# Performance work log

Hardware: AMD Instinct MI355X
Metric: run time of the kernel (lower is better)

Reference implementation:

```python
import jax, jax.numpy as jnp
import numpy as np

N = 50000      # nodes
DIM = 128      # feature dim
H = 4          # heads
C = DIM // H   # per-head channels
E = 800000     # edges (before self-loops)
LRELU_SLOPE = 0.2
LN_EPS = 1e-5


def setup_inputs() -> dict:
    key = jax.random.key(0)
    ks = jax.random.split(key, 12)
    def p(k, shape, scale=0.05):
        return jax.random.normal(k, shape, jnp.float32) * scale
    return {
        "x": jax.random.normal(ks[0], (N, DIM), jnp.float32),
        "edge_index": jax.random.randint(ks[1], (2, E), 0, N),
        "W1": p(ks[2], (DIM, DIM)), "b1": jnp.zeros((DIM,), jnp.float32),
        "att_src1": p(ks[3], (H, C)), "att_dst1": p(ks[4], (H, C)),
        "W2": p(ks[5], (DIM, DIM)), "b2": jnp.zeros((DIM,), jnp.float32),
        "att_src2": p(ks[6], (H, C)), "att_dst2": p(ks[7], (H, C)),
        "gate_W": p(ks[8], (2 * DIM, 2)), "gate_b": jnp.zeros((2,), jnp.float32),
        "ln_gamma": jnp.ones((DIM,), jnp.float32), "ln_beta": jnp.zeros((DIM,), jnp.float32),
    }


def _gat(x, src, dst, W, b, a_src, a_dst):
    # Linear transform, split heads: [N, H, C]
    h = (x @ W).reshape(-1, H, C)
    # Per-node attention logits per head: [N, H]
    e_src = jnp.einsum("nhc,hc->nh", h, a_src)
    e_dst = jnp.einsum("nhc,hc->nh", h, a_dst)
    # Per-edge logits (edge j->i: src=j, dst=i): [E, H]
    e = jax.nn.leaky_relu(e_src[src] + e_dst[dst], LRELU_SLOPE)
    # Segment softmax over edges sharing a destination (self-loops guarantee >=1 edge/node)
    m = jax.ops.segment_max(e, dst, num_segments=N)
    p = jnp.exp(e - m[dst])
    s = jax.ops.segment_sum(p, dst, num_segments=N)
    alpha = p / s[dst]                                   # [E, H]
    # Weighted scatter-add aggregation
    out = jax.ops.segment_sum(h[src] * alpha[..., None], dst, num_segments=N)
    return out.reshape(-1, H * C) + b                    # [N, DIM]


def reference(x, edge_index, W1, b1, att_src1, att_dst1, W2, b2, att_src2, att_dst2,
              gate_W, gate_b, ln_gamma, ln_beta):
    n = x.shape[0]
    loops = jnp.arange(n, dtype=edge_index.dtype)
    src = jnp.concatenate([edge_index[0], loops])  # PyG GATConv add_self_loops=True
    dst = jnp.concatenate([edge_index[1], loops])
    out1 = _gat(x, src, dst, W1, b1, att_src1, att_dst1)
    out2 = _gat(x, src, dst, W2, b2, att_src2, att_dst2)
    gate = jax.nn.softmax(jnp.concatenate([out1, out2], axis=-1) @ gate_W + gate_b, axis=-1)
    out = gate[:, 0:1] * out1 + gate[:, 1:2] * out2
    # residual + LayerNorm (dropout is identity in eval)
    y = x + out
    mu = jnp.mean(y, axis=-1, keepdims=True)
    var = jnp.var(y, axis=-1, keepdims=True)
    return (y - mu) * jax.lax.rsqrt(var + LN_EPS) * ln_gamma + ln_beta
```

## Files before the change

### kernel.cpp

```cpp
#include <hip/hip_runtime.h>
#include <hip/hip_bf16.h>


typedef unsigned short u16;
typedef __bf16 bf16x8 __attribute__((ext_vector_type(8)));
typedef float f32x4 __attribute__((ext_vector_type(4)));

#define LRELU_SLOPE 0.2f
#define LN_EPS 1e-5f
#define SH 8

__device__ __forceinline__ float bfbits(unsigned int hi_bits) {
    union { unsigned int i; float f; } v; v.i = hi_bits; return v.f;
}
__device__ __forceinline__ float bflo(unsigned int u) { return bfbits(u << 16); }
__device__ __forceinline__ float bfhi(unsigned int u) { return bfbits(u & 0xFFFF0000u); }
__device__ __forceinline__ u16 f2bf(float f) {
    union { float f; unsigned int i; } v; v.f = f;
    unsigned int lsb = (v.i >> 16) & 1u;
    v.i += 0x7FFFu + lsb;
    return (u16)(v.i >> 16);
}

__global__ void k_prep(const float* __restrict__ W1, const float* __restrict__ W2,
                       u16* __restrict__ wb, int* __restrict__ deg8,
                       int* __restrict__ gflag, int n) {
    int i = blockIdx.x * 256 + threadIdx.x;
    if (i < 32768) {
        int e = i & 7, chunk = i >> 3;
        int lane = chunk & 63, ks = (chunk >> 6) & 3, t = chunk >> 8;
        int r16 = lane & 15, quad = lane >> 4;
        int colp = t * 16 + r16;
        int k = quad * 8 + ks * 32 + e;
        float v = (colp < 128) ? W1[k * 128 + colp] : W2[k * 128 + (colp - 128)];
        wb[i] = f2bf(v);
    }
    if (i < n) {
#pragma unroll
        for (int x = 0; x < SH; x++) deg8[x * n + i] = 0;
    }
    if (i == 0) *gflag = 0;
}

__global__ __launch_bounds__(256) void k_cg(const float* __restrict__ x,
                                            const u16* __restrict__ wb,
                                            unsigned int* __restrict__ hbp, int n,
                                            const int* __restrict__ ei,
                                            int* __restrict__ deg8,
                                            unsigned int* __restrict__ pk,
                                            int E, int Gg) {
    __shared__ u16 lwb[32768];
    if ((int)blockIdx.x >= Gg) {
        int bid = (int)blockIdx.x - Gg;
#pragma unroll
        for (int it = 0; it < 4; it++) {
            int i = bid * 1024 + it * 256 + threadIdx.x;
            if (i < E) {
                int d = ei[E + i];
                int sh = (i >> 8) & (SH - 1);
                unsigned int r = (unsigned int)atomicAdd(&deg8[sh * n + d], 1);
                pk[i] = (r << 17) | (unsigned int)d;
            }
        }
        return;
    }
    {
        const uint4* g = (const uint4*)wb;
        uint4* l = (uint4*)lwb;
#pragma unroll
        for (int r = 0; r < 16; r++) l[r * 256 + threadIdx.x] = g[r * 256 + threadIdx.x];
    }
    __syncthreads();
    int wave = threadIdx.x >> 6, lane = threadIdx.x & 63;
    int quad = lane >> 4, r16 = lane & 15;
    const u16* bb = lwb + lane * 8;
    for (int strip = 0; strip < 2; strip++) {
        int row = blockIdx.x * 128 + strip * 64 + wave * 16 + r16;
        int arow = (row < n) ? row : n - 1;
        const float* xp = x + (size_t)arow * 128 + quad * 8;
        union { u16 u[8]; bf16x8 b; } ar;
        bf16x8 a[4];
#pragma unroll
        for (int ks = 0; ks < 4; ks++) {
            float4 lo = *(const float4*)(xp + ks * 32);
            float4 hi = *(const float4*)(xp + ks * 32 + 4);
            ar.u[0] = f2bf(lo.x); ar.u[1] = f2bf(lo.y); ar.u[2] = f2bf(lo.z); ar.u[3] = f2bf(lo.w);
            ar.u[4] = f2bf(hi.x); ar.u[5] = f2bf(hi.y); ar.u[6] = f2bf(hi.z); ar.u[7] = f2bf(hi.w);
            a[ks] = ar.b;
        }
        f32x4 acc[16];
#pragma unroll
        for (int t = 0; t < 16; t++) acc[t] = (f32x4){0.f, 0.f, 0.f, 0.f};
#pragma unroll
        for (int t = 0; t < 16; t++) {
#pragma unroll
            for (int ks = 0; ks < 4; ks++) {
                bf16x8 b = *(const bf16x8*)(bb + (t * 4 + ks) * 512);
                acc[t] = __builtin_amdgcn_mfma_f32_16x16x32_bf16(a[ks], b, acc[t], 0, 0, 0);
            }
        }
        int row0 = blockIdx.x * 128 + strip * 64 + wave * 16 + quad * 4;
#pragma unroll
        for (int t = 0; t < 8; t++) {
            int c = t * 16 + r16;
#pragma unroll
            for (int g = 0; g < 4; g++) {
                int gr = row0 + g;
                if (gr < n) {
                    unsigned int pv = ((unsigned int)f2bf(acc[t + 8][g]) << 16) | f2bf(acc[t][g]);
                    hbp[(size_t)gr * 128 + c] = pv;
                }
            }
        }
    }
}

__global__ void k_ss(int* __restrict__ deg8, int* __restrict__ offs,
                     int* __restrict__ bsum, int* __restrict__ gflag,
                     int nb, int n) {
    __shared__ int s[256];
    int t = threadIdx.x;
    int i = blockIdx.x * 256 + t;
    int d[SH];
    int v = 0;
    if (i < n) {
#pragma unroll
        for (int x = 0; x < SH; x++) { d[x] = deg8[x * n + i]; v += d[x]; }
    }
    s[t] = v;
    __syncthreads();
    for (int o = 1; o < 256; o <<= 1) {
        int u = (t >= o) ? s[t - o] : 0;
        __syncthreads();
        s[t] += u;
        __syncthreads();
    }
    int myinc = s[t];
    int total = s[255];
    if (t == 0) {
        bsum[blockIdx.x] = total;
        __threadfence();
        atomicAdd(gflag, 1);
        while (atomicAdd(gflag, 0) < nb) { }
    }
    __syncthreads();
    int bv = (t < (int)blockIdx.x) ? atomicAdd(&bsum[t], 0) : 0;
    s[t] = bv;
    __syncthreads();
    for (int o = 128; o; o >>= 1) {
        if (t < o) s[t] += s[t + o];
        __syncthreads();
    }
    int bp = s[0];
    if (i < n) {
        int e = bp + myinc - v;
        offs[i] = e;
        int run = e;
#pragma unroll
        for (int x = 0; x < SH; x++) { deg8[x * n + i] = run; run += d[x]; }
        if (i == n - 1) offs[n] = e + v;
    }
}

__global__ void k_fl(const int* __restrict__ ei, const int* __restrict__ cursor8,
                     const unsigned int* __restrict__ pk,
                     int* __restrict__ ssrc, int E, int n,
                     const unsigned int* __restrict__ hbp,
                     const float* __restrict__ as1, const float* __restrict__ ad1,
                     const float* __restrict__ as2, const float* __restrict__ ad2,
                     float* __restrict__ es, float* __restrict__ ed, int Gc) {
    if ((int)blockIdx.x >= Gc) {
        int i = ((int)blockIdx.x - Gc) * 256 + threadIdx.x;
        if (i >= n * 4) return;
        int node = i >> 2, head = i & 3;
        const uint4* hv = (const uint4*)(hbp + (size_t)node * 128 + head * 32);
        const float* a1 = as1 + head * 32;
        const float* d1 = ad1 + head * 32;
        const float* a2 = as2 + head * 32;
        const float* d2 = ad2 + head * 32;
        float s1 = 0.f, t1 = 0.f, s2 = 0.f, t2 = 0.f;
#pragma unroll
        for (int q = 0; q < 8; q++) {
            uint4 w = hv[q];
            unsigned int ws[4] = {w.x, w.y, w.z, w.w};
#pragma unroll
            for (int h = 0; h < 4; h++) {
                int c = q * 4 + h;
                float v1 = bflo(ws[h]), v2 = bfhi(ws[h]);
                s1 += v1 * a1[c]; t1 += v1 * d1[c];
                s2 += v2 * a2[c]; t2 += v2 * d2[c];
            }
        }
        *(float2*)(es + node * 8 + head * 2) = make_float2(s1, s2);
        *(float2*)(ed + node * 8 + head * 2) = make_float2(t1, t2);
        return;
    }
#pragma unroll
    for (int it = 0; it < 4; it++) {
        int i = blockIdx.x * 1024 + it * 256 + threadIdx.x;
        if (i < E) {
            int s = ei[i];
            unsigned int v = pk[i];
            int d = (int)(v & 0x1FFFFu);
            int r = (int)(v >> 17);
            int sh = (i >> 8) & (SH - 1);
            ssrc[cursor8[sh * n + d] + r] = s;
        }
    }
}

__device__ __forceinline__ float wred(float v) {
#pragma unroll
    for (int off = 32; off; off >>= 1) v += __shfl_xor(v, off, 64);
    return v;
}

__global__ __launch_bounds__(256) void k_agg(
    const int* __restrict__ offs, const int* __restrict__ ssrc,
    const unsigned int* __restrict__ hbp,
    const float* __restrict__ es, const float* __restrict__ ed,
    const float* __restrict__ b1, const float* __restrict__ b2,
    const float* __restrict__ gW, const float* __restrict__ gb,
    const float* __restrict__ x, const float* __restrict__ gamma,
    const float* __restrict__ beta, float* __restrict__ out, int n) {
    int wave = threadIdx.x >> 6, lane = threadIdx.x & 63;
    int node = blockIdx.x * 4 + wave;
    if (node >= n) return;
    node = __builtin_amdgcn_readfirstlane(node);

    int ca = lane * 2;
    int head = lane >> 4;
    int hh = head * 2;

    float2 edv = *(const float2*)(ed + node * 8 + hh);
    float ed1 = edv.x, ed2 = edv.y;

    float l1 = 0.f, l2 = 0.f;
    float a1a = 0.f, a1b = 0.f, a2a = 0.f, a2b = 0.f;

#define EDGE(sv, q) { \
        float e1 = sv.x + ed1; e1 = fmaxf(e1, LRELU_SLOPE * e1); \
        float e2 = sv.y + ed2; e2 = fmaxf(e2, LRELU_SLOPE * e2); \
        float ww1 = __expf(e1), ww2 = __expf(e2); \
        l1 += ww1; l2 += ww2; \
        a1a += ww1 * bflo(q.x); a1b += ww1 * bflo(q.y); \
        a2a += ww2 * bfhi(q.x); a2b += ww2 * bfhi(q.y); }

    {
        float2 svs = *(const float2*)(es + node * 8 + hh);
        uint2 qs = *(const uint2*)(hbp + (size_t)node * 128 + ca);
        EDGE(svs, qs)
    }

    int beg = offs[node], end = offs[node + 1];
    int k = beg;
    for (; k + 7 < end; k += 8) {
        int jj[8];
#pragma unroll
        for (int u = 0; u < 8; u++) jj[u] = ssrc[k + u];
        float2 sv[8];
#pragma unroll
        for (int u = 0; u < 8; u++) sv[u] = *(const float2*)(es + jj[u] * 8 + hh);
        uint2 qq[8];
#pragma unroll
        for (int u = 0; u < 8; u++) qq[u] = *(const uint2*)(hbp + (size_t)jj[u] * 128 + ca);
#pragma unroll
        for (int u = 0; u < 8; u++) EDGE(sv[u], qq[u])
    }
    if (k + 3 < end) {
        int jj[4];
#pragma unroll
        for (int u = 0; u < 4; u++) jj[u] = ssrc[k + u];
        float2 sv[4];
#pragma unroll
        for (int u = 0; u < 4; u++) sv[u] = *(const float2*)(es + jj[u] * 8 + hh);
        uint2 qq[4];
#pragma unroll
        for (int u = 0; u < 4; u++) qq[u] = *(const uint2*)(hbp + (size_t)jj[u] * 128 + ca);
#pragma unroll
        for (int u = 0; u < 4; u++) EDGE(sv[u], qq[u])
        k += 4;
    }
    for (; k < end; k++) {
        int j = ssrc[k];
        float2 sv = *(const float2*)(es + j * 8 + hh);
        uint2 q = *(const uint2*)(hbp + (size_t)j * 128 + ca);
        EDGE(sv, q)
    }
#undef EDGE

    float2 b1v = *(const float2*)(b1 + ca);
    float2 b2v = *(const float2*)(b2 + ca);
    float r1 = 1.f / l1, r2 = 1.f / l2;
    float o1a = a1a * r1 + b1v.x;
    float o1b = a1b * r1 + b1v.y;
    float o2a = a2a * r2 + b2v.x;
    float o2b = a2b * r2 + b2v.y;

    int cb = ca + 1;
    float2 g1a = *(const float2*)(gW + 2 * ca);
    float2 g1b = *(const float2*)(gW + 2 * cb);
    float2 g2a = *(const float2*)(gW + 2 * (128 + ca));
    float2 g2b = *(const float2*)(gW + 2 * (128 + cb));
    float p0 = o1a * g1a.x + o1b * g1b.x + o2a * g2a.x + o2b * g2b.x;
    float p1 = o1a * g1a.y + o1b * g1b.y + o2a * g2a.y + o2b * g2b.y;
    p0 = wred(p0) + gb[0];
    p1 = wred(p1) + gb[1];
    float mg = fmaxf(p0, p1);
    float eg0 = __expf(p0 - mg), eg1 = __expf(p1 - mg);
    float g0 = eg0 / (eg0 + eg1), g1 = 1.f - g0;

    float2 xv = *(const float2*)(x + (size_t)node * 128 + ca);
    float ya = xv.x + g0 * o1a + g1 * o2a;
    float yb = xv.y + g0 * o1b + g1 * o2b;

    float s  = wred(ya + yb);
    float ss = wred(ya * ya + yb * yb);
    float mean = s * (1.f / 128.f);
    float var  = ss * (1.f / 128.f) - mean * mean;
    float rstd = rsqrtf(var + LN_EPS);
    float2 gv = *(const float2*)(gamma + ca);
    float2 bv = *(const float2*)(beta + ca);
    union { float2 f2; double d; } ov;
    ov.f2.x = (ya - mean) * rstd * gv.x + bv.x;
    ov.f2.y = (yb - mean) * rstd * gv.y + bv.y;
    __builtin_nontemporal_store(ov.d, (double*)(out + (size_t)node * 128 + ca));
}

extern "C" void kernel_launch(void* const* d_in, const int* in_sizes, int n_in,
                              void* d_out, int out_size, void* d_ws, size_t ws_size,
                              hipStream_t stream) {
    const float* x   = (const float*)d_in[0];
    const int*   ei  = (const int*)d_in[1];
    const float* W1  = (const float*)d_in[2];
    const float* b1  = (const float*)d_in[3];
    const float* as1 = (const float*)d_in[4];
    const float* ad1 = (const float*)d_in[5];
    const float* W2  = (const float*)d_in[6];
    const float* b2  = (const float*)d_in[7];
    const float* as2 = (const float*)d_in[8];
    const float* ad2 = (const float*)d_in[9];
    const float* gW  = (const float*)d_in[10];
    const float* gb  = (const float*)d_in[11];
    const float* gamma = (const float*)d_in[12];
    const float* beta  = (const float*)d_in[13];
    float* out = (float*)d_out;

    int n = in_sizes[0] / 128;
    int E = in_sizes[1] / 2;

    char* p = (char*)d_ws;
    auto take = [&](size_t bytes) {
        char* q = p;
        p += (bytes + 255) & ~(size_t)255;
        return (void*)q;
    };
    u16* wb    = (u16*)take((size_t)256 * 128 * 2);
    unsigned int* hbp = (unsigned int*)take((size_t)n * 128 * 4);
    float* es  = (float*)take((size_t)n * 8 * 4);
    float* ed  = (float*)take((size_t)n * 8 * 4);
    int* deg8  = (int*)take((size_t)SH * n * 4);
    int* offs  = (int*)take((size_t)(n + 1) * 4);
    int* bsum  = (int*)take((size_t)256 * 4);
    int* gflag = (int*)take((size_t)256 * 4);
    int* ssrc  = (int*)take((size_t)E * 4);
    unsigned int* pk = (unsigned int*)take((size_t)E * 4);

    int nb  = (n + 255) / 256;
    int Gg  = (n + 127) / 128;
    int Gcc = (E + 1023) / 1024;
    int Gl  = (n * 4 + 255) / 256;

    k_prep<<<nb, 256, 0, stream>>>(W1, W2, wb, deg8, gflag, n);
    k_cg<<<Gg + Gcc, 256, 0, stream>>>(x, wb, hbp, n, ei, deg8, pk, E, Gg);
    k_ss<<<nb, 256, 0, stream>>>(deg8, offs, bsum, gflag, nb, n);
    k_fl<<<Gcc + Gl, 256, 0, stream>>>(ei, deg8, pk, ssrc, E, n, hbp,
                                       as1, ad1, as2, ad2, es, ed, Gcc);
    k_agg<<<(n + 3) / 4, 256, 0, stream>>>(offs, ssrc, hbp, es, ed,
                                           b1, b2, gW, gb, x, gamma, beta, out, n);
}
```

Baseline: 258.3 us.

## Fuse logit computation into GEMM epilogue and reshuffle count/scan kernels

```diff
diff --git a/kernel.cpp b/kernel.cpp
--- a/kernel.cpp
+++ b/kernel.cpp
@@ -22,11 +22,13 @@
     return (u16)(v.i >> 16);
 }
 
-__global__ void k_prep(const float* __restrict__ W1, const float* __restrict__ W2,
-                       u16* __restrict__ wb, int* __restrict__ deg8,
-                       int* __restrict__ gflag, int n) {
-    int i = blockIdx.x * 256 + threadIdx.x;
-    if (i < 32768) {
+__global__ void k_pc(const float* __restrict__ W1, const float* __restrict__ W2,
+                     u16* __restrict__ wb, int* __restrict__ deg8,
+                     int* __restrict__ gflag,
+                     const int* __restrict__ ei, unsigned int* __restrict__ pk,
+                     int E, int n) {
+    if (blockIdx.x < 128) {
+        int i = blockIdx.x * 256 + threadIdx.x;
         int e = i & 7, chunk = i >> 3;
         int lane = chunk & 63, ks = (chunk >> 6) & 3, t = chunk >> 8;
         int r16 = lane & 15, quad = lane >> 4;
@@ -34,33 +36,80 @@
         int k = quad * 8 + ks * 32 + e;
         float v = (colp < 128) ? W1[k * 128 + colp] : W2[k * 128 + (colp - 128)];
         wb[i] = f2bf(v);
-    }
-    if (i < n) {
-#pragma unroll
-        for (int x = 0; x < SH; x++) deg8[x * n + i] = 0;
-    }
-    if (i == 0) *gflag = 0;
+        if (i == 0) *gflag = 0;
+        return;
+    }
+    int bid = (int)blockIdx.x - 128;
+#pragma unroll
+    for (int it = 0; it < 8; it++) {
+        int i = bid * 2048 + it * 256 + threadIdx.x;
+        if (i < E) {
+            int d = ei[E + i];
+            int sh = (i >> 8) & (SH - 1);
+            unsigned int r = (unsigned int)atomicAdd(&deg8[sh * n + d], 1);
+            pk[i] = (r << 17) | (unsigned int)d;
+        }
+    }
 }
 
 __global__ __launch_bounds__(256) void k_cg(const float* __restrict__ x,
                                             const u16* __restrict__ wb,
                                             unsigned int* __restrict__ hbp, int n,
-                                            const int* __restrict__ ei,
+                                            const float* __restrict__ as1,
+                                            const float* __restrict__ ad1,
+                                            const float* __restrict__ as2,
+                                            const float* __restrict__ ad2,
+                                            float* __restrict__ es,
+                                            float* __restrict__ ed,
                                             int* __restrict__ deg8,
-                                            unsigned int* __restrict__ pk,
-                                            int E, int Gg) {
+                                            int* __restrict__ offs,
+                                            int* __restrict__ bsum,
+                                            int* __restrict__ gflag,
+                                            int nb, int Gg) {
     __shared__ u16 lwb[32768];
     if ((int)blockIdx.x >= Gg) {
-        int bid = (int)blockIdx.x - Gg;
-#pragma unroll
-        for (int it = 0; it < 4; it++) {
-            int i = bid * 1024 + it * 256 + threadIdx.x;
-            if (i < E) {
-                int d = ei[E + i];
-                int sh = (i >> 8) & (SH - 1);
-                unsigned int r = (unsigned int)atomicAdd(&deg8[sh * n + d], 1);
-                pk[i] = (r << 17) | (unsigned int)d;
-            }
+        int* si = (int*)lwb;
+        int bblk = (int)blockIdx.x - Gg;
+        int t = threadIdx.x;
+        int i = bblk * 256 + t;
+        int d[SH];
+        int v = 0;
+        if (i < n) {
+#pragma unroll
+            for (int xx = 0; xx < SH; xx++) { d[xx] = deg8[xx * n + i]; v += d[xx]; }
+        }
+        si[t] = v;
+        __syncthreads();
+        for (int o = 1; o < 256; o <<= 1) {
+            int u = (t >= o) ? si[t - o] : 0;
+            __syncthreads();
+            si[t] += u;
+            __syncthreads();
+        }
+        int myinc = si[t];
+        int total = si[255];
+        if (t == 0) {
+            bsum[bblk] = total;
+            __threadfence();
+            atomicAdd(gflag, 1);
+            while (atomicAdd(gflag, 0) < nb) __builtin_amdgcn_s_sleep(8);
+        }
+        __syncthreads();
+        int bv = (t < bblk) ? atomicAdd(&bsum[t], 0) : 0;
+        si[t] = bv;
+        __syncthreads();
+        for (int o = 128; o; o >>= 1) {
+            if (t < o) si[t] += si[t + o];
+            __syncthreads();
+        }
+        int bp = si[0];
+        if (i < n) {
+            int e = bp + myinc - v;
+            offs[i] = e;
+            int run = e;
+#pragma unroll
+            for (int xx = 0; xx < SH; xx++) { deg8[xx * n + i] = run; run += d[xx]; }
+            if (i == n - 1) offs[n] = e + v;
         }
         return;
     }
@@ -74,6 +123,14 @@
     int wave = threadIdx.x >> 6, lane = threadIdx.x & 63;
     int quad = lane >> 4, r16 = lane & 15;
     const u16* bb = lwb + lane * 8;
+    float2 aS1[4], aD1[4], aS2[4], aD2[4];
+#pragma unroll
+    for (int h = 0; h < 4; h++) {
+        aS1[h] = make_float2(as1[h * 32 + r16], as1[h * 32 + 16 + r16]);
+        aD1[h] = make_float2(ad1[h * 32 + r16], ad1[h * 32 + 16 + r16]);
+        aS2[h] = make_float2(as2[h * 32 + r16], as2[h * 32 + 16 + r16]);
+        aD2[h] = make_float2(ad2[h * 32 + r16], ad2[h * 32 + 16 + r16]);
+    }
     for (int strip = 0; strip < 2; strip++) {
         int row = blockIdx.x * 128 + strip * 64 + wave * 16 + r16;
         int arow = (row < n) ? row : n - 1;
@@ -112,89 +169,56 @@
                 }
             }
         }
-    }
-}
-
-__global__ void k_ss(int* __restrict__ deg8, int* __restrict__ offs,
-                     int* __restrict__ bsum, int* __restrict__ gflag,
-                     int nb, int n) {
-    __shared__ int s[256];
-    int t = threadIdx.x;
-    int i = blockIdx.x * 256 + t;
-    int d[SH];
-    int v = 0;
-    if (i < n) {
-#pragma unroll
-        for (int x = 0; x < SH; x++) { d[x] = deg8[x * n + i]; v += d[x]; }
-    }
-    s[t] = v;
-    __syncthreads();
-    for (int o = 1; o < 256; o <<= 1) {
-        int u = (t >= o) ? s[t - o] : 0;
-        __syncthreads();
-        s[t] += u;
-        __syncthreads();
-    }
-    int myinc = s[t];
-    int total = s[255];
-    if (t == 0) {
-        bsum[blockIdx.x] = total;
-        __threadfence();
-        atomicAdd(gflag, 1);
-        while (atomicAdd(gflag, 0) < nb) { }
-    }
-    __syncthreads();
-    int bv = (t < (int)blockIdx.x) ? atomicAdd(&bsum[t], 0) : 0;
-    s[t] = bv;
-    __syncthreads();
-    for (int o = 128; o; o >>= 1) {
-        if (t < o) s[t] += s[t + o];
-        __syncthreads();
-    }
-    int bp = s[0];
-    if (i < n) {
-        int e = bp + myinc - v;
-        offs[i] = e;
-        int run = e;
-#pragma unroll
-        for (int x = 0; x < SH; x++) { deg8[x * n + i] = run; run += d[x]; }
-        if (i == n - 1) offs[n] = e + v;
+#pragma unroll
+        for (int g = 0; g < 4; g++) {
+            int grow = row0 + g;
+            float v[16];
+#pragma unroll
+            for (int h = 0; h < 4; h++) {
+                float x1 = acc[2 * h][g],     y1 = acc[2 * h + 1][g];
+                float x2 = acc[8 + 2 * h][g], y2 = acc[8 + 2 * h + 1][g];
+                v[h * 2 + 0]     = x1 * aS1[h].x + y1 * aS1[h].y;
+                v[h * 2 + 1]     = x2 * aS2[h].x + y2 * aS2[h].y;
+                v[8 + h * 2 + 0] = x1 * aD1[h].x + y1 * aD1[h].y;
+                v[8 + h * 2 + 1] = x2 * aD2[h].x + y2 * aD2[h].y;
+            }
+            int b0 = r16 & 1, b1 = r16 & 2, b2 = r16 & 4, b3 = r16 & 8;
+            float w8[8];
+#pragma unroll
+            for (int k2 = 0; k2 < 8; k2++) {
+                float keep = b0 ? v[2 * k2 + 1] : v[2 * k2];
+                float send = b0 ? v[2 * k2]     : v[2 * k2 + 1];
+                w8[k2] = keep + __shfl_xor(send, 1, 64);
+            }
+            float w4v[4];
+#pragma unroll
+            for (int k2 = 0; k2 < 4; k2++) {
+                float keep = b1 ? w8[2 * k2 + 1] : w8[2 * k2];
+                float send = b1 ? w8[2 * k2]     : w8[2 * k2 + 1];
+                w4v[k2] = keep + __shfl_xor(send, 2, 64);
+            }
+            float w2v[2];
+#pragma unroll
+            for (int k2 = 0; k2 < 2; k2++) {
+                float keep = b2 ? w4v[2 * k2 + 1] : w4v[2 * k2];
+                float send = b2 ? w4v[2 * k2]     : w4v[2 * k2 + 1];
+                w2v[k2] = keep + __shfl_xor(send, 4, 64);
+            }
+            float keep = b3 ? w2v[1] : w2v[0];
+            float send = b3 ? w2v[0] : w2v[1];
+            float wv = keep + __shfl_xor(send, 8, 64);
+            if (grow < n) {
+                float* dstp = (r16 < 8) ? (es + (size_t)grow * 8 + r16)
+                                        : (ed + (size_t)grow * 8 + (r16 - 8));
+                *dstp = wv;
+            }
+        }
     }
 }
 
 __global__ void k_fl(const int* __restrict__ ei, const int* __restrict__ cursor8,
                      const unsigned int* __restrict__ pk,
-                     int* __restrict__ ssrc, int E, int n,
-                     const unsigned int* __restrict__ hbp,
-                     const float* __restrict__ as1, const float* __restrict__ ad1,
-                     const float* __restrict__ as2, const float* __restrict__ ad2,
-                     float* __restrict__ es, float* __restrict__ ed, int Gc) {
-    if ((int)blockIdx.x >= Gc) {
-        int i = ((int)blockIdx.x - Gc) * 256 + threadIdx.x;
-        if (i >= n * 4) return;
-        int node = i >> 2, head = i & 3;
-        const uint4* hv = (const uint4*)(hbp + (size_t)node * 128 + head * 32);
-        const float* a1 = as1 + head * 32;
-        const float* d1 = ad1 + head * 32;
-        const float* a2 = as2 + head * 32;
-        const float* d2 = ad2 + head * 32;
-        float s1 = 0.f, t1 = 0.f, s2 = 0.f, t2 = 0.f;
-#pragma unroll
-        for (int q = 0; q < 8; q++) {
-            uint4 w = hv[q];
-            unsigned int ws[4] = {w.x, w.y, w.z, w.w};
-#pragma unroll
-            for (int h = 0; h < 4; h++) {
-                int c = q * 4 + h;
-                float v1 = bflo(ws[h]), v2 = bfhi(ws[h]);
-                s1 += v1 * a1[c]; t1 += v1 * d1[c];
-                s2 += v2 * a2[c]; t2 += v2 * d2[c];
-            }
-        }
-        *(float2*)(es + node * 8 + head * 2) = make_float2(s1, s2);
-        *(float2*)(ed + node * 8 + head * 2) = make_float2(t1, t2);
-        return;
-    }
+                     int* __restrict__ ssrc, int E, int n) {
 #pragma unroll
     for (int it = 0; it < 4; it++) {
         int i = blockIdx.x * 1024 + it * 256 + threadIdx.x;
@@ -254,32 +278,17 @@
 
     int beg = offs[node], end = offs[node + 1];
     int k = beg;
-    for (; k + 7 < end; k += 8) {
-        int jj[8];
-#pragma unroll
-        for (int u = 0; u < 8; u++) jj[u] = ssrc[k + u];
-        float2 sv[8];
-#pragma unroll
-        for (int u = 0; u < 8; u++) sv[u] = *(const float2*)(es + jj[u] * 8 + hh);
-        uint2 qq[8];
-#pragma unroll
-        for (int u = 0; u < 8; u++) qq[u] = *(const uint2*)(hbp + (size_t)jj[u] * 128 + ca);
-#pragma unroll
-        for (int u = 0; u < 8; u++) EDGE(sv[u], qq[u])
-    }
-    if (k + 3 < end) {
-        int jj[4];
-#pragma unroll
-        for (int u = 0; u < 4; u++) jj[u] = ssrc[k + u];
-        float2 sv[4];
-#pragma unroll
-        for (int u = 0; u < 4; u++) sv[u] = *(const float2*)(es + jj[u] * 8 + hh);
-        uint2 qq[4];
-#pragma unroll
-        for (int u = 0; u < 4; u++) qq[u] = *(const uint2*)(hbp + (size_t)jj[u] * 128 + ca);
-#pragma unroll
-        for (int u = 0; u < 4; u++) EDGE(sv[u], qq[u])
-        k += 4;
+    for (; k + 3 < end; k += 4) {
+        int j0 = ssrc[k], j1 = ssrc[k + 1], j2 = ssrc[k + 2], j3 = ssrc[k + 3];
+        float2 s0 = *(const float2*)(es + j0 * 8 + hh);
+        float2 s1 = *(const float2*)(es + j1 * 8 + hh);
+        float2 s2 = *(const float2*)(es + j2 * 8 + hh);
+        float2 s3 = *(const float2*)(es + j3 * 8 + hh);
+        uint2 q0 = *(const uint2*)(hbp + (size_t)j0 * 128 + ca);
+        uint2 q1 = *(const uint2*)(hbp + (size_t)j1 * 128 + ca);
+        uint2 q2 = *(const uint2*)(hbp + (size_t)j2 * 128 + ca);
+        uint2 q3 = *(const uint2*)(hbp + (size_t)j3 * 128 + ca);
+        EDGE(s0, q0) EDGE(s1, q1) EDGE(s2, q2) EDGE(s3, q3)
     }
     for (; k < end; k++) {
         int j = ssrc[k];
@@ -368,14 +377,14 @@
 
     int nb  = (n + 255) / 256;
     int Gg  = (n + 127) / 128;
-    int Gcc = (E + 1023) / 1024;
-    int Gl  = (n * 4 + 255) / 256;
-
-    k_prep<<<nb, 256, 0, stream>>>(W1, W2, wb, deg8, gflag, n);
-    k_cg<<<Gg + Gcc, 256, 0, stream>>>(x, wb, hbp, n, ei, deg8, pk, E, Gg);
-    k_ss<<<nb, 256, 0, stream>>>(deg8, offs, bsum, gflag, nb, n);
-    k_fl<<<Gcc + Gl, 256, 0, stream>>>(ei, deg8, pk, ssrc, E, n, hbp,
-                                       as1, ad1, as2, ad2, es, ed, Gcc);
+    int Gc8 = (E + 2047) / 2048;
+    int Gso = (E + 1023) / 1024;
+
+    hipMemsetAsync(deg8, 0, (size_t)SH * n * 4, stream);
+    k_pc<<<128 + Gc8, 256, 0, stream>>>(W1, W2, wb, deg8, gflag, ei, pk, E, n);
+    k_cg<<<Gg + nb, 256, 0, stream>>>(x, wb, hbp, n, as1, ad1, as2, ad2,
+                                      es, ed, deg8, offs, bsum, gflag, nb, Gg);
+    k_fl<<<Gso, 256, 0, stream>>>(ei, deg8, pk, ssrc, E, n);
     k_agg<<<(n + 3) / 4, 256, 0, stream>>>(offs, ssrc, hbp, es, ed,
                                            b1, b2, gW, gb, x, gamma, beta, out, n);
 }
```

Result: no change. 256.0 us (-0.9%).
